# Optimization experiments

Measured on AMD Instinct MI355X. Metric: run time of the kernel, lower is better.

The kernel has to match this reference:

```python
import jax, jax.numpy as jnp
import numpy as np

W_WIN = 5  # sliding rank-pooling window (init arg w)
GRAY_W = np.array([0.2989, 0.587, 0.114], dtype=np.float32)  # torchvision Grayscale


def _window_weight_matrix(T, w):
    # Wmat[t, s] = rank-pooling weight of frame s inside window starting at t.
    # Window t covers frames t..t+N-1 with N = min(w, T-t); weights 2*(j+1)-N-1.
    M = np.zeros((T, T), dtype=np.float32)
    for t in range(T):
        N = min(w, T - t)
        for j in range(N):
            M[t, t + j] = 2.0 * (j + 1) - N - 1
    return jnp.asarray(M)


def setup_inputs() -> dict:
    key = jax.random.key(0)
    x = jax.random.normal(key, (8, 3, 64, 224, 224), dtype=jnp.float32)
    return {"x": x}


def reference(x):
    B, C, T, H, W = x.shape
    Wmat = _window_weight_matrix(T, W_WIN)  # [T, T], banded (bandwidth W_WIN)
    # Weighted sum over each sliding window: re[t] = sum_s Wmat[t,s] * x[:,:,s]
    re = jnp.einsum('ts,bcshw->tbchw', Wmat, x)  # [T,B,C,H,W]
    re = jax.nn.gelu(re, approximate=False)  # torch F.gelu is exact (erf)
    # Global (over B,C,H,W) min-subtract then max-normalize, per window t
    mn = re.min(axis=(1, 2, 3, 4), keepdims=True)
    re = re - mn
    mx = re.max(axis=(1, 2, 3, 4), keepdims=True)
    denom = jnp.where(mx != 0, mx, mx + 1e-5)
    re = re / denom
    # Grayscale: ITU-R 601 weighted channel sum -> 1 channel
    gray = jnp.einsum('tbchw,c->tbhw', re, jnp.asarray(GRAY_W, re.dtype))
    out = jnp.transpose(gray, (1, 0, 2, 3))[:, None]  # [B,1,T,H,W]
    mask = jnp.zeros((B, 1, W_WIN - 1, H, W), dtype=out.dtype)
    return jnp.concatenate([mask, out], axis=2)  # [B,1,T+w-1,H,W]
```

## Files before the change

kernel.cpp:

```cpp
#include <hip/hip_runtime.h>

#define HW 50176
#define TT 64
#define NB1 1568
#define NB2 1568
#define NB3 26656
#define SUMW 0.9999f

__device__ __forceinline__ float gelu_erf(float x) {
    return 0.5f * x * (1.0f + erff(0.70710678f * x));
}
__device__ __forceinline__ float fast_rcp(float v) {
    float r; asm("v_rcp_f32 %0, %1" : "=v"(r) : "v"(v)); return r;
}
__device__ __forceinline__ float gelu_fast(float x) {
    float x2 = x * x;
    float e = exp2f(-x * fmaf(0.1029433f, x2, 2.3022078f));
    return x * fast_rcp(1.0f + e);
}
__device__ __forceinline__ unsigned encf(float f) {
    unsigned u = __float_as_uint(f);
    return (u & 0x80000000u) ? ~u : (u | 0x80000000u);
}
__device__ __forceinline__ float decf(unsigned u) {
    unsigned b = (u & 0x80000000u) ? (u ^ 0x80000000u) : ~u;
    return __uint_as_float(b);
}
__device__ __forceinline__ unsigned pk_min_f16(unsigned a, unsigned b) {
    unsigned r; asm("v_pk_min_f16 %0, %1, %2" : "=v"(r) : "v"(a), "v"(b)); return r;
}
__device__ __forceinline__ unsigned pack2(float lo, float hi) {
    auto p = __builtin_amdgcn_cvt_pkrtz(lo, hi);
    return __builtin_bit_cast(unsigned, p);
}
__device__ __forceinline__ unsigned min4(float4 re) {
    return pk_min_f16(pk_min_f16(pack2(re.x, -re.x), pack2(re.y, -re.y)),
                      pk_min_f16(pack2(re.z, -re.z), pack2(re.w, -re.w)));
}
__device__ __forceinline__ float4 re_full(float4 w0, float4 w1, float4 w3, float4 w4) {
    float4 r;
    r.x = fmaf(4.f, w4.x - w0.x, 2.f * (w3.x - w1.x));
    r.y = fmaf(4.f, w4.y - w0.y, 2.f * (w3.y - w1.y));
    r.z = fmaf(4.f, w4.z - w0.z, 2.f * (w3.z - w1.z));
    r.w = fmaf(4.f, w4.w - w0.w, 2.f * (w3.w - w1.w));
    return r;
}

__global__ void k_init(unsigned* __restrict__ g) {
    int i = threadIdx.x;
    g[i] = (i < TT) ? 0xFFFFFFFFu : 0u;
}

template<bool WGS>
__global__ __launch_bounds__(256, 4) void k_pass1(const float* __restrict__ x,
                                                  unsigned* __restrict__ gmm,
                                                  unsigned short* __restrict__ gs) {
    __shared__ unsigned smin[16], smax[16];
    const int tid = threadIdx.x;
    if (tid < 16) { smin[tid] = 0xFFFFFFFFu; smax[tid] = 0u; }
    __syncthreads();

    const int bid   = blockIdx.x;
    const int b     = bid / 196;
    const int rem   = bid - b * 196;
    const int tc    = rem / 49;
    const int hwblk = rem - tc * 49;
    const int t0    = tc * 16;
    const int hw    = (hwblk * 256 + tid) * 4;
    const float* xa = x + ((size_t)(b * 3 + 0) * TT + t0) * (size_t)HW + hw;
    const float* xb = x + ((size_t)(b * 3 + 1) * TT + t0) * (size_t)HW + hw;
    const float* xc = x + ((size_t)(b * 3 + 2) * TT + t0) * (size_t)HW + hw;
    unsigned short* gp = gs + ((size_t)b * TT + t0) * (size_t)HW + hw;

    unsigned acc[16];
    #pragma unroll
    for (int j = 0; j < 16; ++j) acc[j] = 0x7BFF7BFFu;

    #define LDA(f) (*(const float4*)(xa + (size_t)(f) * HW))
    #define LDB(f) (*(const float4*)(xb + (size_t)(f) * HW))
    #define LDC(f) (*(const float4*)(xc + (size_t)(f) * HW))

    auto step = [&](float4 ra, float4 rb, float4 rc, int j) {
        unsigned m = pk_min_f16(pk_min_f16(min4(ra), min4(rb)), min4(rc));
        acc[j] = pk_min_f16(acc[j], m);
        if constexpr (WGS) {
            float4 g;
            g.x = fmaf(0.114f, gelu_fast(rc.x), fmaf(0.587f, gelu_fast(rb.x), 0.2989f * gelu_fast(ra.x)));
            g.y = fmaf(0.114f, gelu_fast(rc.y), fmaf(0.587f, gelu_fast(rb.y), 0.2989f * gelu_fast(ra.y)));
            g.z = fmaf(0.114f, gelu_fast(rc.z), fmaf(0.587f, gelu_fast(rb.z), 0.2989f * gelu_fast(ra.z)));
            g.w = fmaf(0.114f, gelu_fast(rc.w), fmaf(0.587f, gelu_fast(rb.w), 0.2989f * gelu_fast(ra.w)));
            uint2 st; st.x = pack2(g.x, g.y); st.y = pack2(g.z, g.w);
            *(uint2*)(gp + (size_t)j * HW) = st;
        }
    };

    float4 a0 = LDA(0), a1 = LDA(1), a2 = LDA(2), a3 = LDA(3), a4 = LDA(4), pa = LDA(5);
    float4 b0 = LDB(0), b1 = LDB(1), b2 = LDB(2), b3 = LDB(3), b4 = LDB(4), pb = LDB(5);
    float4 c0 = LDC(0), c1 = LDC(1), c2 = LDC(2), c3 = LDC(3), c4 = LDC(4), pc = LDC(5);

    if (tc < 3) {
        #pragma unroll
        for (int j = 0; j < 16; ++j) {
            step(re_full(a0, a1, a3, a4), re_full(b0, b1, b3, b4), re_full(c0, c1, c3, c4), j);
            a0 = a1; a1 = a2; a2 = a3; a3 = a4; a4 = pa;
            b0 = b1; b1 = b2; b2 = b3; b3 = b4; b4 = pb;
            c0 = c1; c1 = c2; c2 = c3; c3 = c4; c4 = pc;
            if (j < 14) { pa = LDA(j + 6); pb = LDB(j + 6); pc = LDC(j + 6); }
        }
    } else {
        #pragma unroll
        for (int j = 0; j < 16; ++j) {
            float4 ra, rb, rc;
            if (j < 12) {
                ra = re_full(a0, a1, a3, a4); rb = re_full(b0, b1, b3, b4); rc = re_full(c0, c1, c3, c4);
            } else if (j == 12) {
                ra.x = fmaf(3.f, a3.x - a0.x, a2.x - a1.x); ra.y = fmaf(3.f, a3.y - a0.y, a2.y - a1.y);
                ra.z = fmaf(3.f, a3.z - a0.z, a2.z - a1.z); ra.w = fmaf(3.f, a3.w - a0.w, a2.w - a1.w);
                rb.x = fmaf(3.f, b3.x - b0.x, b2.x - b1.x); rb.y = fmaf(3.f, b3.y - b0.y, b2.y - b1.y);
                rb.z = fmaf(3.f, b3.z - b0.z, b2.z - b1.z); rb.w = fmaf(3.f, b3.w - b0.w, b2.w - b1.w);
                rc.x = fmaf(3.f, c3.x - c0.x, c2.x - c1.x); rc.y = fmaf(3.f, c3.y - c0.y, c2.y - c1.y);
                rc.z = fmaf(3.f, c3.z - c0.z, c2.z - c1.z); rc.w = fmaf(3.f, c3.w - c0.w, c2.w - c1.w);
            } else if (j == 13) {
                ra.x = 2.f*(a2.x-a0.x); ra.y = 2.f*(a2.y-a0.y); ra.z = 2.f*(a2.z-a0.z); ra.w = 2.f*(a2.w-a0.w);
                rb.x = 2.f*(b2.x-b0.x); rb.y = 2.f*(b2.y-b0.y); rb.z = 2.f*(b2.z-b0.z); rb.w = 2.f*(b2.w-b0.w);
                rc.x = 2.f*(c2.x-c0.x); rc.y = 2.f*(c2.y-c0.y); rc.z = 2.f*(c2.z-c0.z); rc.w = 2.f*(c2.w-c0.w);
            } else if (j == 14) {
                ra.x = a1.x-a0.x; ra.y = a1.y-a0.y; ra.z = a1.z-a0.z; ra.w = a1.w-a0.w;
                rb.x = b1.x-b0.x; rb.y = b1.y-b0.y; rb.z = b1.z-b0.z; rb.w = b1.w-b0.w;
                rc.x = c1.x-c0.x; rc.y = c1.y-c0.y; rc.z = c1.z-c0.z; rc.w = c1.w-c0.w;
            } else {
                ra.x=ra.y=ra.z=ra.w=0.f; rb=ra; rc=ra;
            }
            step(ra, rb, rc, j);
            a0 = a1; a1 = a2; a2 = a3; a3 = a4; a4 = pa;
            b0 = b1; b1 = b2; b2 = b3; b3 = b4; b4 = pb;
            c0 = c1; c1 = c2; c2 = c3; c3 = c4; c4 = pc;
            if (j < 10) { pa = LDA(j + 6); pb = LDB(j + 6); pc = LDC(j + 6); }
        }
    }
    #undef LDA
    #undef LDB
    #undef LDC

    const int lane = tid & 63;
    unsigned keep = 0x7BFF7BFFu;
    #pragma unroll
    for (int j = 0; j < 16; ++j) {
        unsigned a = acc[j];
        #pragma unroll
        for (int off = 32; off; off >>= 1)
            a = pk_min_f16(a, (unsigned)__shfl_xor((int)a, off, 64));
        if (lane == j) keep = a;
    }

    if (lane < 16) {
        union { unsigned u; _Float16 h[2]; } cv; cv.u = keep;
        const float amin = (float)cv.h[0];
        const float amax = -(float)cv.h[1];
        const float g0 = gelu_erf(amin), g1 = gelu_erf(amax);
        const float gmax = fmaxf(g0, g1);
        const float XSTAR = -0.7517916f;
        float gmin;
        if (amin >= XSTAR)      gmin = g0;
        else if (amax <= XSTAR) gmin = g1;
        else                    gmin = fminf(gelu_erf(XSTAR), fminf(g0, g1));
        atomicMin(&smin[lane], encf(gmin));
        atomicMax(&smax[lane], encf(gmax));
    }
    __syncthreads();
    if (tid < 16)            atomicMin(&gmm[t0 + tid], smin[tid]);
    else if (tid < 32)       atomicMax(&gmm[TT + t0 + tid - 16], smax[tid - 16]);
}

__global__ void k_consts(const unsigned* __restrict__ gmm, float* __restrict__ ab) {
    int t = threadIdx.x;
    float mn = decf(gmm[t]);
    float mx = decf(gmm[TT + t]) - mn;
    float inv = 1.0f / ((mx != 0.0f) ? mx : 1e-5f);
    ab[t]      = inv;
    ab[TT + t] = -mn * SUMW * inv;
}

__global__ __launch_bounds__(256) void k_pass3(const unsigned short* __restrict__ gs,
                                               const float* __restrict__ ab,
                                               float* __restrict__ out) {
    const int bid = blockIdx.x;
    const int b  = bid / (68 * 49);
    const int r  = bid - b * (68 * 49);
    const int t  = r / 49;
    const int hb = r - t * 49;
    const int px = (hb * 256 + threadIdx.x) * 4;
    float* op = out + ((size_t)b * 68 + t) * (size_t)HW + px;
    if (t < 4) { *(float4*)op = make_float4(0.f, 0.f, 0.f, 0.f); return; }
    const int tm = t - 4;
    uint2 v = *(const uint2*)(gs + ((size_t)b * TT + tm) * (size_t)HW + px);
    const float A = ab[tm], Bv = ab[TT + tm];
    union { unsigned u; _Float16 h[2]; } lo, hi; lo.u = v.x; hi.u = v.y;
    float4 o;
    o.x = fmaf((float)lo.h[0], A, Bv);
    o.y = fmaf((float)lo.h[1], A, Bv);
    o.z = fmaf((float)hi.h[0], A, Bv);
    o.w = fmaf((float)hi.h[1], A, Bv);
    *(float4*)op = o;
}

__global__ __launch_bounds__(256) void k_pass2_direct(const float* __restrict__ x,
                                                      const float* __restrict__ ab,
                                                      float* __restrict__ out) {
    __shared__ float sA[TT], sB[TT];
    const int tid = threadIdx.x;
    if (tid < TT)          sA[tid] = ab[tid];
    else if (tid < 2 * TT) sB[tid - TT] = ab[tid];
    __syncthreads();

    const int pix = blockIdx.x * 256 + tid;
    const int b  = pix / HW;
    const int hw = pix - b * HW;
    const float* x0 = x + (size_t)(b * 3) * (TT * (size_t)HW) + hw;
    const float* x1 = x0 + (size_t)TT * HW;
    const float* x2 = x1 + (size_t)TT * HW;
    float* op = out + (size_t)b * (68 * (size_t)HW) + hw;

    op[0] = 0.f; op[HW] = 0.f; op[2 * (size_t)HW] = 0.f; op[3 * (size_t)HW] = 0.f;
    op += 4 * (size_t)HW;

    float a0 = x0[0], a1 = x0[HW], a2 = x0[2*HW], a3 = x0[3*HW], a4 = x0[4*HW];
    float b0 = x1[0], b1 = x1[HW], b2 = x1[2*HW], b3 = x1[3*HW], b4 = x1[4*HW];
    float c0 = x2[0], c1 = x2[HW], c2 = x2[2*HW], c3 = x2[3*HW], c4 = x2[4*HW];

    auto emit = [&](int t, float ra, float rb, float rc) {
        float gsv = 0.2989f * gelu_erf(ra) + 0.587f * gelu_erf(rb) + 0.114f * gelu_erf(rc);
        op[(size_t)t * HW] = fmaf(gsv, sA[t], sB[t]);
    };

    for (int t = 0; t < 59; ++t) {
        emit(t, 4.f*(a4-a0) + 2.f*(a3-a1), 4.f*(b4-b0) + 2.f*(b3-b1), 4.f*(c4-c0) + 2.f*(c3-c1));
        a0=a1; a1=a2; a2=a3; a3=a4; a4 = x0[(size_t)(t+5)*HW];
        b0=b1; b1=b2; b2=b3; b3=b4; b4 = x1[(size_t)(t+5)*HW];
        c0=c1; c1=c2; c2=c3; c3=c4; c4 = x2[(size_t)(t+5)*HW];
    }
    emit(59, 4.f*(a4-a0) + 2.f*(a3-a1), 4.f*(b4-b0) + 2.f*(b3-b1), 4.f*(c4-c0) + 2.f*(c3-c1));
    a0=a1; a1=a2; a2=a3; a3=a4; b0=b1; b1=b2; b2=b3; b3=b4; c0=c1; c1=c2; c2=c3; c3=c4;
    emit(60, 3.f*(a3-a0) + (a2-a1), 3.f*(b3-b0) + (b2-b1), 3.f*(c3-c0) + (c2-c1));
    a0=a1; a1=a2; a2=a3; b0=b1; b1=b2; b2=b3; c0=c1; c1=c2; c2=c3;
    emit(61, 2.f*(a2-a0), 2.f*(b2-b0), 2.f*(c2-c0));
    a0=a1; a1=a2; b0=b1; b1=b2; c0=c1; c1=c2;
    emit(62, a1-a0, b1-b0, c1-c0);
    op[63 * (size_t)HW] = sB[63];
}

extern "C" void kernel_launch(void* const* d_in, const int* in_sizes, int n_in,
                              void* d_out, int out_size, void* d_ws, size_t ws_size,
                              hipStream_t stream) {
    const float* x = (const float*)d_in[0];
    float* out = (float*)d_out;
    unsigned* gmm = (unsigned*)d_ws;
    float* ab = (float*)d_ws + 128;
    unsigned short* gs = (unsigned short*)((char*)d_ws + 1024);
    const size_t need = 1024 + (size_t)8 * TT * (size_t)HW * 2;

    k_init<<<1, 128, 0, stream>>>(gmm);
    if (ws_size >= need) {
        k_pass1<true><<<NB1, 256, 0, stream>>>(x, gmm, gs);
        k_consts<<<1, 64, 0, stream>>>(gmm, ab);
        k_pass3<<<NB3, 256, 0, stream>>>(gs, ab, out);
    } else {
        k_pass1<false><<<NB1, 256, 0, stream>>>(x, gmm, nullptr);
        k_consts<<<1, 64, 0, stream>>>(gmm, ab);
        k_pass2_direct<<<NB2, 256, 0, stream>>>(x, ab, out);
    }
}
```

Before: 131.8 us.

## Narrow pass1 to float2 per thread, fold consts into pass3, memset init

Pass1 now handles 2 pixels per thread instead of 4, doubling the block count and raising launch_bounds occupancy to 6, with the aim of cutting register pressure and hiding latency better. The per-window scale constants are computed inline in pass3 from the global min/max, which removes the k_consts launch. Pass3 now processes 7 float4 per thread with far fewer blocks. The init kernel is replaced by two hipMemsetAsync calls. Risks: memsets can cost as much as a tiny kernel, and narrower loads may reduce per-request memory efficiency.

```diff
diff --git a/kernel.cpp b/kernel.cpp
--- a/kernel.cpp
+++ b/kernel.cpp
@@ -1,10 +1,11 @@
 #include <hip/hip_runtime.h>
 
 #define HW 50176
+#define HW2 25088
+#define HW4 12544
 #define TT 64
-#define NB1 1568
-#define NB2 1568
-#define NB3 26656
+#define NB1 3136
+#define NB3 3808
 #define SUMW 0.9999f
 
 __device__ __forceinline__ float gelu_erf(float x) {
@@ -33,75 +34,62 @@
     auto p = __builtin_amdgcn_cvt_pkrtz(lo, hi);
     return __builtin_bit_cast(unsigned, p);
 }
-__device__ __forceinline__ unsigned min4(float4 re) {
-    return pk_min_f16(pk_min_f16(pack2(re.x, -re.x), pack2(re.y, -re.y)),
-                      pk_min_f16(pack2(re.z, -re.z), pack2(re.w, -re.w)));
-}
-__device__ __forceinline__ float4 re_full(float4 w0, float4 w1, float4 w3, float4 w4) {
-    float4 r;
+__device__ __forceinline__ unsigned mm2(float2 r) {
+    return pk_min_f16(pack2(r.x, -r.x), pack2(r.y, -r.y));
+}
+__device__ __forceinline__ float2 re_full2(float2 w0, float2 w1, float2 w3, float2 w4) {
+    float2 r;
     r.x = fmaf(4.f, w4.x - w0.x, 2.f * (w3.x - w1.x));
     r.y = fmaf(4.f, w4.y - w0.y, 2.f * (w3.y - w1.y));
-    r.z = fmaf(4.f, w4.z - w0.z, 2.f * (w3.z - w1.z));
-    r.w = fmaf(4.f, w4.w - w0.w, 2.f * (w3.w - w1.w));
     return r;
 }
 
-__global__ void k_init(unsigned* __restrict__ g) {
-    int i = threadIdx.x;
-    g[i] = (i < TT) ? 0xFFFFFFFFu : 0u;
-}
-
 template<bool WGS>
-__global__ __launch_bounds__(256, 4) void k_pass1(const float* __restrict__ x,
+__global__ __launch_bounds__(256, 6) void k_pass1(const float* __restrict__ x,
                                                   unsigned* __restrict__ gmm,
-                                                  unsigned short* __restrict__ gs) {
+                                                  unsigned* __restrict__ gs) {
     __shared__ unsigned smin[16], smax[16];
     const int tid = threadIdx.x;
     if (tid < 16) { smin[tid] = 0xFFFFFFFFu; smax[tid] = 0u; }
     __syncthreads();
 
-    const int bid   = blockIdx.x;
-    const int b     = bid / 196;
-    const int rem   = bid - b * 196;
-    const int tc    = rem / 49;
-    const int hwblk = rem - tc * 49;
-    const int t0    = tc * 16;
-    const int hw    = (hwblk * 256 + tid) * 4;
+    const int bid = blockIdx.x;
+    const int b   = bid / 392;
+    const int rem = bid - b * 392;
+    const int tc  = rem / 98;
+    const int hwb = rem - tc * 98;
+    const int t0  = tc * 16;
+    const int hw  = (hwb * 256 + tid) * 2;
     const float* xa = x + ((size_t)(b * 3 + 0) * TT + t0) * (size_t)HW + hw;
     const float* xb = x + ((size_t)(b * 3 + 1) * TT + t0) * (size_t)HW + hw;
     const float* xc = x + ((size_t)(b * 3 + 2) * TT + t0) * (size_t)HW + hw;
-    unsigned short* gp = gs + ((size_t)b * TT + t0) * (size_t)HW + hw;
+    unsigned* gp = gs + ((size_t)b * TT + t0) * (size_t)HW2 + (hwb * 256 + tid);
 
     unsigned acc[16];
     #pragma unroll
     for (int j = 0; j < 16; ++j) acc[j] = 0x7BFF7BFFu;
 
-    #define LDA(f) (*(const float4*)(xa + (size_t)(f) * HW))
-    #define LDB(f) (*(const float4*)(xb + (size_t)(f) * HW))
-    #define LDC(f) (*(const float4*)(xc + (size_t)(f) * HW))
-
-    auto step = [&](float4 ra, float4 rb, float4 rc, int j) {
-        unsigned m = pk_min_f16(pk_min_f16(min4(ra), min4(rb)), min4(rc));
-        acc[j] = pk_min_f16(acc[j], m);
+    #define LDA(f) (*(const float2*)(xa + (size_t)(f) * HW))
+    #define LDB(f) (*(const float2*)(xb + (size_t)(f) * HW))
+    #define LDC(f) (*(const float2*)(xc + (size_t)(f) * HW))
+
+    auto step = [&](float2 ra, float2 rb, float2 rc, int j) {
+        acc[j] = pk_min_f16(acc[j], pk_min_f16(pk_min_f16(mm2(ra), mm2(rb)), mm2(rc)));
         if constexpr (WGS) {
-            float4 g;
-            g.x = fmaf(0.114f, gelu_fast(rc.x), fmaf(0.587f, gelu_fast(rb.x), 0.2989f * gelu_fast(ra.x)));
-            g.y = fmaf(0.114f, gelu_fast(rc.y), fmaf(0.587f, gelu_fast(rb.y), 0.2989f * gelu_fast(ra.y)));
-            g.z = fmaf(0.114f, gelu_fast(rc.z), fmaf(0.587f, gelu_fast(rb.z), 0.2989f * gelu_fast(ra.z)));
-            g.w = fmaf(0.114f, gelu_fast(rc.w), fmaf(0.587f, gelu_fast(rb.w), 0.2989f * gelu_fast(ra.w)));
-            uint2 st; st.x = pack2(g.x, g.y); st.y = pack2(g.z, g.w);
-            *(uint2*)(gp + (size_t)j * HW) = st;
+            float gx = fmaf(0.114f, gelu_fast(rc.x), fmaf(0.587f, gelu_fast(rb.x), 0.2989f * gelu_fast(ra.x)));
+            float gy = fmaf(0.114f, gelu_fast(rc.y), fmaf(0.587f, gelu_fast(rb.y), 0.2989f * gelu_fast(ra.y)));
+            gp[(size_t)j * HW2] = pack2(gx, gy);
         }
     };
 
-    float4 a0 = LDA(0), a1 = LDA(1), a2 = LDA(2), a3 = LDA(3), a4 = LDA(4), pa = LDA(5);
-    float4 b0 = LDB(0), b1 = LDB(1), b2 = LDB(2), b3 = LDB(3), b4 = LDB(4), pb = LDB(5);
-    float4 c0 = LDC(0), c1 = LDC(1), c2 = LDC(2), c3 = LDC(3), c4 = LDC(4), pc = LDC(5);
+    float2 a0 = LDA(0), a1 = LDA(1), a2 = LDA(2), a3 = LDA(3), a4 = LDA(4), pa = LDA(5);
+    float2 b0 = LDB(0), b1 = LDB(1), b2 = LDB(2), b3 = LDB(3), b4 = LDB(4), pb = LDB(5);
+    float2 c0 = LDC(0), c1 = LDC(1), c2 = LDC(2), c3 = LDC(3), c4 = LDC(4), pc = LDC(5);
 
     if (tc < 3) {
         #pragma unroll
         for (int j = 0; j < 16; ++j) {
-            step(re_full(a0, a1, a3, a4), re_full(b0, b1, b3, b4), re_full(c0, c1, c3, c4), j);
+            step(re_full2(a0, a1, a3, a4), re_full2(b0, b1, b3, b4), re_full2(c0, c1, c3, c4), j);
             a0 = a1; a1 = a2; a2 = a3; a3 = a4; a4 = pa;
             b0 = b1; b1 = b2; b2 = b3; b3 = b4; b4 = pb;
             c0 = c1; c1 = c2; c2 = c3; c3 = c4; c4 = pc;
@@ -110,26 +98,23 @@
     } else {
         #pragma unroll
         for (int j = 0; j < 16; ++j) {
-            float4 ra, rb, rc;
+            float2 ra, rb, rc;
             if (j < 12) {
-                ra = re_full(a0, a1, a3, a4); rb = re_full(b0, b1, b3, b4); rc = re_full(c0, c1, c3, c4);
+                ra = re_full2(a0, a1, a3, a4); rb = re_full2(b0, b1, b3, b4); rc = re_full2(c0, c1, c3, c4);
             } else if (j == 12) {
                 ra.x = fmaf(3.f, a3.x - a0.x, a2.x - a1.x); ra.y = fmaf(3.f, a3.y - a0.y, a2.y - a1.y);
-                ra.z = fmaf(3.f, a3.z - a0.z, a2.z - a1.z); ra.w = fmaf(3.f, a3.w - a0.w, a2.w - a1.w);
                 rb.x = fmaf(3.f, b3.x - b0.x, b2.x - b1.x); rb.y = fmaf(3.f, b3.y - b0.y, b2.y - b1.y);
-                rb.z = fmaf(3.f, b3.z - b0.z, b2.z - b1.z); rb.w = fmaf(3.f, b3.w - b0.w, b2.w - b1.w);
                 rc.x = fmaf(3.f, c3.x - c0.x, c2.x - c1.x); rc.y = fmaf(3.f, c3.y - c0.y, c2.y - c1.y);
-                rc.z = fmaf(3.f, c3.z - c0.z, c2.z - c1.z); rc.w = fmaf(3.f, c3.w - c0.w, c2.w - c1.w);
             } else if (j == 13) {
-                ra.x = 2.f*(a2.x-a0.x); ra.y = 2.f*(a2.y-a0.y); ra.z = 2.f*(a2.z-a0.z); ra.w = 2.f*(a2.w-a0.w);
-                rb.x = 2.f*(b2.x-b0.x); rb.y = 2.f*(b2.y-b0.y); rb.z = 2.f*(b2.z-b0.z); rb.w = 2.f*(b2.w-b0.w);
-                rc.x = 2.f*(c2.x-c0.x); rc.y = 2.f*(c2.y-c0.y); rc.z = 2.f*(c2.z-c0.z); rc.w = 2.f*(c2.w-c0.w);
+                ra.x = 2.f*(a2.x-a0.x); ra.y = 2.f*(a2.y-a0.y);
+                rb.x = 2.f*(b2.x-b0.x); rb.y = 2.f*(b2.y-b0.y);
+                rc.x = 2.f*(c2.x-c0.x); rc.y = 2.f*(c2.y-c0.y);
             } else if (j == 14) {
-                ra.x = a1.x-a0.x; ra.y = a1.y-a0.y; ra.z = a1.z-a0.z; ra.w = a1.w-a0.w;
-                rb.x = b1.x-b0.x; rb.y = b1.y-b0.y; rb.z = b1.z-b0.z; rb.w = b1.w-b0.w;
-                rc.x = c1.x-c0.x; rc.y = c1.y-c0.y; rc.z = c1.z-c0.z; rc.w = c1.w-c0.w;
+                ra.x = a1.x-a0.x; ra.y = a1.y-a0.y;
+                rb.x = b1.x-b0.x; rb.y = b1.y-b0.y;
+                rc.x = c1.x-c0.x; rc.y = c1.y-c0.y;
             } else {
-                ra.x=ra.y=ra.z=ra.w=0.f; rb=ra; rc=ra;
+                ra.x = ra.y = 0.f; rb = ra; rc = ra;
             }
             step(ra, rb, rc, j);
             a0 = a1; a1 = a2; a2 = a3; a3 = a4; a4 = pa;
@@ -172,6 +157,43 @@
     else if (tid < 32)       atomicMax(&gmm[TT + t0 + tid - 16], smax[tid - 16]);
 }
 
+__global__ __launch_bounds__(256) void k_pass3(const unsigned* __restrict__ gs,
+                                               const unsigned* __restrict__ gmm,
+                                               float* __restrict__ out) {
+    const int bid = blockIdx.x;
+    const int b   = bid / 476;
+    const int r   = bid - b * 476;
+    const int t   = r / 7;
+    const int seg = r - t * 7;
+    const int base4 = seg * 1792 + threadIdx.x;
+    float4* op = (float4*)out + ((size_t)b * 68 + t) * HW4 + base4;
+
+    if (t < 4) {
+        float4 z = make_float4(0.f, 0.f, 0.f, 0.f);
+        #pragma unroll
+        for (int k = 0; k < 7; ++k) op[k * 256] = z;
+        return;
+    }
+    const int tm = t - 4;
+    const float mn = decf(gmm[tm]);
+    const float mx = decf(gmm[TT + tm]) - mn;
+    const float inv = fast_rcp((mx != 0.f) ? mx : 1e-5f);
+    const float A = inv, Bv = -mn * SUMW * inv;
+
+    const uint2* gpp = (const uint2*)gs + ((size_t)b * TT + tm) * HW4 + base4;
+    #pragma unroll
+    for (int k = 0; k < 7; ++k) {
+        uint2 v = gpp[k * 256];
+        union { unsigned u; _Float16 h[2]; } lo, hi; lo.u = v.x; hi.u = v.y;
+        float4 o;
+        o.x = fmaf((float)lo.h[0], A, Bv);
+        o.y = fmaf((float)lo.h[1], A, Bv);
+        o.z = fmaf((float)hi.h[0], A, Bv);
+        o.w = fmaf((float)hi.h[1], A, Bv);
+        op[k * 256] = o;
+    }
+}
+
 __global__ void k_consts(const unsigned* __restrict__ gmm, float* __restrict__ ab) {
     int t = threadIdx.x;
     float mn = decf(gmm[t]);
@@ -179,29 +201,6 @@
     float inv = 1.0f / ((mx != 0.0f) ? mx : 1e-5f);
     ab[t]      = inv;
     ab[TT + t] = -mn * SUMW * inv;
-}
-
-__global__ __launch_bounds__(256) void k_pass3(const unsigned short* __restrict__ gs,
-                                               const float* __restrict__ ab,
-                                               float* __restrict__ out) {
-    const int bid = blockIdx.x;
-    const int b  = bid / (68 * 49);
-    const int r  = bid - b * (68 * 49);
-    const int t  = r / 49;
-    const int hb = r - t * 49;
-    const int px = (hb * 256 + threadIdx.x) * 4;
-    float* op = out + ((size_t)b * 68 + t) * (size_t)HW + px;
-    if (t < 4) { *(float4*)op = make_float4(0.f, 0.f, 0.f, 0.f); return; }
-    const int tm = t - 4;
-    uint2 v = *(const uint2*)(gs + ((size_t)b * TT + tm) * (size_t)HW + px);
-    const float A = ab[tm], Bv = ab[TT + tm];
-    union { unsigned u; _Float16 h[2]; } lo, hi; lo.u = v.x; hi.u = v.y;
-    float4 o;
-    o.x = fmaf((float)lo.h[0], A, Bv);
-    o.y = fmaf((float)lo.h[1], A, Bv);
-    o.z = fmaf((float)hi.h[0], A, Bv);
-    o.w = fmaf((float)hi.h[1], A, Bv);
-    *(float4*)op = o;
 }
 
 __global__ __launch_bounds__(256) void k_pass2_direct(const float* __restrict__ x,
@@ -256,17 +255,18 @@
     float* out = (float*)d_out;
     unsigned* gmm = (unsigned*)d_ws;
     float* ab = (float*)d_ws + 128;
-    unsigned short* gs = (unsigned short*)((char*)d_ws + 1024);
+    unsigned* gs = (unsigned*)((char*)d_ws + 1024);
     const size_t need = 1024 + (size_t)8 * TT * (size_t)HW * 2;
 
-    k_init<<<1, 128, 0, stream>>>(gmm);
+    hipMemsetAsync(gmm, 0xFF, TT * sizeof(unsigned), stream);
+    hipMemsetAsync(gmm + TT, 0x00, TT * sizeof(unsigned), stream);
+
     if (ws_size >= need) {
         k_pass1<true><<<NB1, 256, 0, stream>>>(x, gmm, gs);
-        k_consts<<<1, 64, 0, stream>>>(gmm, ab);
-        k_pass3<<<NB3, 256, 0, stream>>>(gs, ab, out);
+        k_pass3<<<NB3, 256, 0, stream>>>(gs, gmm, out);
     } else {
         k_pass1<false><<<NB1, 256, 0, stream>>>(x, gmm, nullptr);
         k_consts<<<1, 64, 0, stream>>>(gmm, ab);
-        k_pass2_direct<<<NB2, 256, 0, stream>>>(x, ab, out);
-    }
-}
+        k_pass2_direct<<<1568, 256, 0, stream>>>(x, ab, out);
+    }
+}
```

Measured after the change: 132.5 us. No clear change (+0.6%).
